# Optimization experiments

Measured on AMD Instinct MI355X. Metric: run time of the kernel, lower is better.

The kernel has to match this reference:

```python
import jax, jax.numpy as jnp
import numpy as np

B, H, S, DK, DV = 2, 16, 2048, 64, 64


def setup_inputs() -> dict:
    key = jax.random.key(0)
    kq, kk, kv, km = jax.random.split(key, 4)
    Q = jax.random.normal(kq, (B, H, S, DK), dtype=jnp.float32)
    K = jax.random.normal(kk, (B, H, S, DK), dtype=jnp.float32)
    V = jax.random.normal(kv, (B, H, S, DV), dtype=jnp.float32)
    attn_mask = jax.random.randint(km, (B, H, S, S), 0, 2).astype(jnp.bool_)
    return {
        "Q": Q, "K": K, "V": V, "attn_mask": attn_mask,
        "d_model": 1024, "n_layers": 6, "n_heads": H,
        "d_k": DK, "d_v": DV, "d_ff": 4096,
    }


def reference(Q, K, V, attn_mask, d_model, n_layers, n_heads, d_k, d_v, d_ff):
    # scores: [B, H, S, S] = Q K^T / sqrt(d_k)
    scale = 1.0 / np.sqrt(d_k).astype(np.float32)
    scores = jnp.einsum('bhqd,bhkd->bhqk', Q, K) * scale
    scores = jnp.where(attn_mask, jnp.asarray(-1e9, scores.dtype), scores)
    attn = jax.nn.softmax(scores, axis=-1)
    context = jnp.einsum('bhqk,bhkd->bhqd', attn, V)
    return (context, attn)
```

## Files before the change

### kernel.cpp

```cpp
#include <hip/hip_runtime.h>
#include <hip/hip_fp16.h>

#define S_LEN 2048
#define DKV 64
#define NBH 32
#define CTX_ELEMS ((size_t)NBH * S_LEN * DKV)

using half8 = __attribute__((ext_vector_type(8))) _Float16;
using half4 = __attribute__((ext_vector_type(4))) _Float16;
using f32x4 = __attribute__((ext_vector_type(4))) float;
using u32x4 = __attribute__((ext_vector_type(4))) unsigned int;

#define MFMA16x32(a, b, c) __builtin_amdgcn_mfma_f32_16x16x32_f16((a), (b), (c), 0, 0, 0)

__global__ void detect_mask_kernel(const unsigned char* __restrict__ mask,
                                   int* __restrict__ flag) {
  __shared__ int nz0s, nzos;
  if (threadIdx.x == 0) { nz0s = 0; nzos = 0; }
  __syncthreads();
  const u32x4* m = (const u32x4*)mask;
  unsigned int a0 = 0, ao = 0;
  for (int i = threadIdx.x; i < 8192; i += 512) {
    u32x4 v = m[i];
#pragma unroll
    for (int j = 0; j < 4; j++) {
      a0 |= v[j] & 0xffu;
      ao |= v[j] & 0xffffff00u;
    }
  }
  if (a0) atomicAdd(&nz0s, 1);
  if (ao) atomicAdd(&nzos, 1);
  __syncthreads();
  if (threadIdx.x == 0) *flag = (nz0s > 0 && nzos > 0) ? 0 : 1;
}

#define PACK_B 2048
#define CONV_B 128
#define NF4 (NBH * S_LEN * DKV / 4)

__global__ void fused_pre_kernel(const void* __restrict__ maskv,
                                 const int* __restrict__ flag,
                                 unsigned int* __restrict__ bits,
                                 const float* __restrict__ Q, _Float16* __restrict__ QH,
                                 const float* __restrict__ K, _Float16* __restrict__ KH,
                                 const float* __restrict__ V, _Float16* __restrict__ VT) {
  __shared__ unsigned char nib[256];
  __shared__ _Float16 t[64][68];
  const int bidx = blockIdx.x;
  const int tid = threadIdx.x;

  if (bidx < PACK_B) {
    const bool w4 = (*flag) != 0;
    const unsigned int* m32 = (const unsigned int*)maskv;
    if (w4) {
      const int w = tid >> 6;
      const int lane = tid & 63;
      for (int it = 0; it < 64; ++it) {
        const size_t wb = ((size_t)bidx * 64 + it) * 1024 + (size_t)w * 256;
        u32x4 v = __builtin_nontemporal_load((const u32x4*)(m32 + wb + lane * 4));
        unsigned int x = ((v[0] ? 1u : 0u) | (v[1] ? 2u : 0u) |
                          (v[2] ? 4u : 0u) | (v[3] ? 8u : 0u)) << ((lane & 7) * 4);
        x |= __shfl_xor(x, 1, 64);
        x |= __shfl_xor(x, 2, 64);
        x |= __shfl_xor(x, 4, 64);
        if ((lane & 7) == 0)
          bits[(wb >> 5) + (lane >> 3)] = x;
      }
    } else {
      for (int it = 0; it < 64; ++it) {
        const size_t e0 = ((size_t)bidx * 64 + it) * 1024;
        const size_t ei = e0 + (size_t)tid * 4;
        unsigned int b = __builtin_nontemporal_load(m32 + (ei >> 2));
        unsigned int nv = ((b & 0xffu) ? 1u : 0u) | ((b & 0xff00u) ? 2u : 0u) |
                          ((b & 0xff0000u) ? 4u : 0u) | ((b & 0xff000000u) ? 8u : 0u);
        __syncthreads();
        nib[tid] = (unsigned char)nv;
        __syncthreads();
        if (tid < 32) {
          unsigned int dw = 0;
#pragma unroll
          for (int tt = 0; tt < 8; ++tt)
            dw |= ((unsigned int)nib[tid * 8 + tt]) << (tt * 4);
          bits[(e0 >> 5) + tid] = dw;
        }
      }
    }
  } else if (bidx < PACK_B + 2 * CONV_B) {
    const bool isQ = bidx < PACK_B + CONV_B;
    const int cb = bidx - (isQ ? PACK_B : PACK_B + CONV_B);
    const float* src = isQ ? Q : K;
    _Float16* dst = isQ ? QH : KH;
    const float scale = isQ ? 0.125f : 1.0f;
    for (int i = cb * 256 + tid; i < NF4; i += CONV_B * 256) {
      f32x4 v = *(const f32x4*)(src + (size_t)i * 4);
      half4 h;
#pragma unroll
      for (int j = 0; j < 4; j++) h[j] = (_Float16)(v[j] * scale);
      *(half4*)(dst + (size_t)i * 4) = h;
    }
  } else {
    const int tIdx = bidx - (PACK_B + 2 * CONV_B);
    const int bh = tIdx >> 5;
    const int k0 = (tIdx & 31) * 64;
    const float* Vb = V + ((size_t)bh * S_LEN + k0) * DKV;
#pragma unroll
    for (int it = 0; it < 4; it++) {
      int idx = tid + it * 256;
      int kl = idx >> 4;
      int dq = (idx & 15) * 4;
      f32x4 v = *(const f32x4*)(Vb + (size_t)kl * DKV + dq);
#pragma unroll
      for (int j = 0; j < 4; j++) t[kl][dq + j] = (_Float16)v[j];
    }
    __syncthreads();
    _Float16* VTb = VT + (size_t)bh * DKV * S_LEN;
#pragma unroll
    for (int it = 0; it < 4; it++) {
      int idx = tid + it * 256;
      int d = idx >> 4;
      int kq = (idx & 15) * 4;
      half4 h;
#pragma unroll
      for (int j = 0; j < 4; j++) h[j] = t[kq + j][d];
      *(half4*)(VTb + (size_t)d * S_LEN + k0 + kq) = h;
    }
  }
}

#define LOADF(S, KT) { \
  const _Float16* kp_ = Kb + ((size_t)((KT) * 32 + c)) * DKV + g * 8; \
  k00##S = *(const half8*)kp_; \
  k01##S = *(const half8*)(kp_ + 32); \
  k10##S = *(const half8*)(kp_ + 16 * DKV); \
  k11##S = *(const half8*)(kp_ + 16 * DKV + 32); }

#define P1SUB(KT, S) { \
  unsigned int mwA[4], mwB[4]; \
  _Pragma("unroll") for (int e = 0; e < 4; e++) { \
    mwA[e] = bq[(size_t)(g * 4 + e) * (S_LEN / 32) + (KT)]; \
    mwB[e] = bq[(size_t)(16 + g * 4 + e) * (S_LEN / 32) + (KT)]; } \
  f32x4 acA0 = (f32x4)0.0f, acA1 = (f32x4)0.0f; \
  f32x4 acB0 = (f32x4)0.0f, acB1 = (f32x4)0.0f; \
  acA0 = MFMA16x32(aA0, k00##S, acA0); \
  acA0 = MFMA16x32(aA1, k01##S, acA0); \
  acB0 = MFMA16x32(aB0, k00##S, acB0); \
  acB0 = MFMA16x32(aB1, k01##S, acB0); \
  acA1 = MFMA16x32(aA0, k10##S, acA1); \
  acA1 = MFMA16x32(aA1, k11##S, acA1); \
  acB1 = MFMA16x32(aB0, k10##S, acB1); \
  acB1 = MFMA16x32(aB1, k11##S, acB1); \
  _Pragma("unroll") for (int e = 0; e < 4; e++) { \
    float pA0 = ((mwA[e] >> c) & 1u) ? 0.0f : __expf(acA0[e]); \
    float pA1 = ((mwA[e] >> (16 + c)) & 1u) ? 0.0f : __expf(acA1[e]); \
    float pB0 = ((mwB[e] >> c) & 1u) ? 0.0f : __expf(acB0[e]); \
    float pB1 = ((mwB[e] >> (16 + c)) & 1u) ? 0.0f : __expf(acB1[e]); \
    ZsA[e] += pA0 + pA1; \
    ZsB[e] += pB0 + pB1; } }

#define P2SUB(KT, S) { \
  unsigned int mwA[4], mwB[4]; \
  _Pragma("unroll") for (int e = 0; e < 4; e++) { \
    mwA[e] = bq[(size_t)(g * 4 + e) * (S_LEN / 32) + (KT)]; \
    mwB[e] = bq[(size_t)(16 + g * 4 + e) * (S_LEN / 32) + (KT)]; } \
  half8 vb0 = *(const half8*)(Vb + (size_t)(0 * 16 + c) * S_LEN + (KT) * 32 + g * 8); \
  half8 vb1 = *(const half8*)(Vb + (size_t)(1 * 16 + c) * S_LEN + (KT) * 32 + g * 8); \
  half8 vb2 = *(const half8*)(Vb + (size_t)(2 * 16 + c) * S_LEN + (KT) * 32 + g * 8); \
  half8 vb3 = *(const half8*)(Vb + (size_t)(3 * 16 + c) * S_LEN + (KT) * 32 + g * 8); \
  f32x4 acA0 = (f32x4)0.0f, acA1 = (f32x4)0.0f; \
  f32x4 acB0 = (f32x4)0.0f, acB1 = (f32x4)0.0f; \
  acA0 = MFMA16x32(aA0, k00##S, acA0); \
  acA0 = MFMA16x32(aA1, k01##S, acA0); \
  acB0 = MFMA16x32(aB0, k00##S, acB0); \
  acB0 = MFMA16x32(aB1, k01##S, acB0); \
  acA1 = MFMA16x32(aA0, k10##S, acA1); \
  acA1 = MFMA16x32(aA1, k11##S, acA1); \
  acB1 = MFMA16x32(aB0, k10##S, acB1); \
  acB1 = MFMA16x32(aB1, k11##S, acB1); \
  _Pragma("unroll") for (int e = 0; e < 4; e++) { \
    float pA0 = ((mwA[e] >> c) & 1u) ? 0.0f : __expf(acA0[e] - lZA[e]); \
    float pA1 = ((mwA[e] >> (16 + c)) & 1u) ? 0.0f : __expf(acA1[e] - lZA[e]); \
    float pB0 = ((mwB[e] >> c) & 1u) ? 0.0f : __expf(acB0[e] - lZB[e]); \
    float pB1 = ((mwB[e] >> (16 + c)) & 1u) ? 0.0f : __expf(acB1[e] - lZB[e]); \
    pbuf[w][g * 4 + e][c] = (_Float16)pA0; \
    pbuf[w][g * 4 + e][16 + c] = (_Float16)pA1; \
    pbuf[w][16 + g * 4 + e][c] = (_Float16)pB0; \
    pbuf[w][16 + g * 4 + e][16 + c] = (_Float16)pB1; } \
  half8 paA = *(const half8*)&pbuf[w][c][g * 8]; \
  half8 paB = *(const half8*)&pbuf[w][16 + c][g * 8]; \
  _Pragma("unroll") for (int s = 0; s < 4; s++) { \
    const int r = (lane >> 3) + s * 8; \
    const int c4 = (lane & 7) * 4; \
    half4 h = *(const half4*)&pbuf[w][r][c4]; \
    f32x4 o; \
    _Pragma("unroll") for (int j = 0; j < 4; j++) o[j] = (float)h[j]; \
    __builtin_nontemporal_store(o, \
        (f32x4*)(attn_base + (size_t)r * S_LEN + (KT) * 32 + c4)); } \
  ctxA[0] = MFMA16x32(paA, vb0, ctxA[0]); \
  ctxB[0] = MFMA16x32(paB, vb0, ctxB[0]); \
  ctxA[1] = MFMA16x32(paA, vb1, ctxA[1]); \
  ctxB[1] = MFMA16x32(paB, vb1, ctxB[1]); \
  ctxA[2] = MFMA16x32(paA, vb2, ctxA[2]); \
  ctxB[2] = MFMA16x32(paB, vb2, ctxB[2]); \
  ctxA[3] = MFMA16x32(paA, vb3, ctxA[3]); \
  ctxB[3] = MFMA16x32(paB, vb3, ctxB[3]); }

__global__ __launch_bounds__(512, 2)
void attn_v10_kernel(const _Float16* __restrict__ QH, const _Float16* __restrict__ KH,
                     const _Float16* __restrict__ VT, const unsigned int* __restrict__ bits,
                     float* __restrict__ out) {
  __shared__ __align__(16) _Float16 pbuf[8][32][40];
  __shared__ float zbuf[4][2][32];
  __shared__ __align__(16) float cbuf[4][32][64];

  const int tid = threadIdx.x;
  const int w = tid >> 6;
  const int lane = tid & 63;
  const int g = lane >> 4;
  const int c = lane & 15;
  const int tb = w >> 1;
  const int half = w & 1;

  const int phys = blockIdx.x;
  const int orig = (phys & 7) * 64 + (phys >> 3);
  const int tile = orig * 4 + tb;
  const int bh = tile >> 6;
  const int q0 = (tile & 63) << 5;

  const _Float16* qpA = QH + ((size_t)(bh * S_LEN + q0 + c)) * DKV + g * 8;
  const half8 aA0 = *(const half8*)qpA;
  const half8 aA1 = *(const half8*)(qpA + 32);
  const _Float16* qpB = qpA + 16 * DKV;
  const half8 aB0 = *(const half8*)qpB;
  const half8 aB1 = *(const half8*)(qpB + 32);

  const _Float16* Kb = KH + (size_t)bh * S_LEN * DKV;
  const unsigned int* bq = bits + ((size_t)(bh * S_LEN + q0)) * (S_LEN / 32);

  float ZsA[4] = {0.0f, 0.0f, 0.0f, 0.0f};
  float ZsB[4] = {0.0f, 0.0f, 0.0f, 0.0f};

  const int kt0 = half * 32;
  half8 k00a, k01a, k10a, k11a, k00b, k01b, k10b, k11b;

  LOADF(a, kt0);
  for (int sp = 0; sp < 16; ++sp) {
    const int s0 = kt0 + sp * 2;
    LOADF(b, s0 + 1);
    P1SUB(s0, a);
    if (sp < 15) LOADF(a, s0 + 2);
    P1SUB(s0 + 1, b);
  }

#pragma unroll
  for (int off = 1; off < 16; off <<= 1) {
#pragma unroll
    for (int e = 0; e < 4; e++) {
      ZsA[e] += __shfl_xor(ZsA[e], off, 64);
      ZsB[e] += __shfl_xor(ZsB[e], off, 64);
    }
  }
  if (c == 0) {
#pragma unroll
    for (int e = 0; e < 4; e++) {
      zbuf[tb][half][g * 4 + e] = ZsA[e];
      zbuf[tb][half][16 + g * 4 + e] = ZsB[e];
    }
  }
  __syncthreads();
  float lZA[4], lZB[4];
#pragma unroll
  for (int e = 0; e < 4; e++) {
    lZA[e] = __logf(zbuf[tb][0][g * 4 + e] + zbuf[tb][1][g * 4 + e]);
    lZB[e] = __logf(zbuf[tb][0][16 + g * 4 + e] + zbuf[tb][1][16 + g * 4 + e]);
  }

  f32x4 ctxA[4], ctxB[4];
#pragma unroll
  for (int nn = 0; nn < 4; nn++) { ctxA[nn] = (f32x4)0.0f; ctxB[nn] = (f32x4)0.0f; }

  const _Float16* Vb = VT + (size_t)bh * DKV * S_LEN;
  float* attn_base = out + CTX_ELEMS + ((size_t)(bh * S_LEN + q0)) * S_LEN;

  LOADF(a, kt0);
  for (int sp = 0; sp < 16; ++sp) {
    const int s0 = kt0 + sp * 2;
    LOADF(b, s0 + 1);
    P2SUB(s0, a);
    if (sp < 15) LOADF(a, s0 + 2);
    P2SUB(s0 + 1, b);
  }

  __syncthreads();
  if (half == 1) {
#pragma unroll
    for (int nn = 0; nn < 4; nn++) {
#pragma unroll
      for (int e = 0; e < 4; e++) {
        cbuf[tb][g * 4 + e][nn * 16 + c] = ctxA[nn][e];
        cbuf[tb][16 + g * 4 + e][nn * 16 + c] = ctxB[nn][e];
      }
    }
  }
  __syncthreads();
  if (half == 0) {
    float* cb = out + ((size_t)(bh * S_LEN + q0)) * DKV;
#pragma unroll
    for (int nn = 0; nn < 4; nn++) {
#pragma unroll
      for (int e = 0; e < 4; e++) {
        float vA = ctxA[nn][e] + cbuf[tb][g * 4 + e][nn * 16 + c];
        float vB = ctxB[nn][e] + cbuf[tb][16 + g * 4 + e][nn * 16 + c];
        __builtin_nontemporal_store(vA, cb + (size_t)(g * 4 + e) * DKV + nn * 16 + c);
        __builtin_nontemporal_store(vB, cb + (size_t)(16 + g * 4 + e) * DKV + nn * 16 + c);
      }
    }
  }
}

__global__ __launch_bounds__(512, 1)
void attn_slow_kernel(const float* __restrict__ Q, const float* __restrict__ K,
                      const float* __restrict__ V, const void* __restrict__ maskv,
                      float* __restrict__ out, const int* __restrict__ flag) {
  __shared__ __align__(16) unsigned char smem[16 * 2056 * 2];
  __shared__ float redm[8][16];
  __shared__ float reds[8][16];
  _Float16 (*P)[2056] = (_Float16 (*)[2056])smem;

  const int bh = blockIdx.y;
  const int q0 = blockIdx.x << 4;
  const int tid = threadIdx.x;
  const int w = tid >> 6;
  const int lane = tid & 63;
  const int g = lane >> 4;
  const int c = lane & 15;
  const int k0 = w << 8;

  const bool mask_w = (*flag) != 0;
  const unsigned char* m8 = (const unsigned char*)maskv;
  const unsigned int* m32 = (const unsigned int*)maskv;

  const float* Qb = Q + ((size_t)bh * S_LEN + q0) * DKV;
  const float* Kb = K + (size_t)bh * S_LEN * DKV;
  const float* Vb = V + (size_t)bh * S_LEN * DKV;
  const size_t mbase = ((size_t)bh * S_LEN + q0) * S_LEN;
  float* ctx_out = out + ((size_t)bh * S_LEN + q0) * DKV;
  float* attn_out = out + CTX_ELEMS + mbase;

  half8 a0, a1;
  {
    const float* qrow = Qb + (size_t)c * DKV + g * 8;
    f32x4 x0 = *(const f32x4*)(qrow);
    f32x4 x1 = *(const f32x4*)(qrow + 4);
    f32x4 y0 = *(const f32x4*)(qrow + 32);
    f32x4 y1 = *(const f32x4*)(qrow + 36);
#pragma unroll
    for (int j = 0; j < 4; j++) {
      a0[j] = (_Float16)x0[j]; a0[4 + j] = (_Float16)x1[j];
      a1[j] = (_Float16)y0[j]; a1[4 + j] = (_Float16)y1[j];
    }
  }

  f32x4 acc[16];
#pragma unroll
  for (int n = 0; n < 16; n++) acc[n] = (f32x4)0.0f;
#pragma unroll
  for (int n = 0; n < 16; n++) {
    const float* kr = Kb + (size_t)(k0 + n * 16 + c) * DKV + g * 8;
    f32x4 x0 = *(const f32x4*)(kr);
    f32x4 x1 = *(const f32x4*)(kr + 4);
    f32x4 y0 = *(const f32x4*)(kr + 32);
    f32x4 y1 = *(const f32x4*)(kr + 36);
    half8 b0, b1;
#pragma unroll
    for (int j = 0; j < 4; j++) {
      b0[j] = (_Float16)x0[j]; b0[4 + j] = (_Float16)x1[j];
      b1[j] = (_Float16)y0[j]; b1[4 + j] = (_Float16)y1[j];
    }
    acc[n] = MFMA16x32(a0, b0, acc[n]);
    acc[n] = MFMA16x32(a1, b1, acc[n]);
  }

  float mx[4] = {-1e9f, -1e9f, -1e9f, -1e9f};
#pragma unroll
  for (int n = 0; n < 16; n++) {
    const int kc = k0 + n * 16 + c;
#pragma unroll
    for (int e = 0; e < 4; e++) {
      const size_t mi = mbase + (size_t)(g * 4 + e) * S_LEN + kc;
      bool masked;
      if (mask_w) masked = (__builtin_nontemporal_load(&m32[mi]) != 0u);
      else        masked = (__builtin_nontemporal_load(&m8[mi]) != 0);
      float s = masked ? -1e9f : acc[n][e] * 0.125f;
      acc[n][e] = s;
      mx[e] = fmaxf(mx[e], s);
    }
  }
#pragma unroll
  for (int off = 1; off < 16; off <<= 1) {
#pragma unroll
    for (int e = 0; e < 4; e++)
      mx[e] = fmaxf(mx[e], __shfl_xor(mx[e], off, 64));
  }
  if (c == 0) {
#pragma unroll
    for (int e = 0; e < 4; e++) redm[w][g * 4 + e] = mx[e];
  }
  __syncthreads();
  float m[4], sm[4];
#pragma unroll
  for (int e = 0; e < 4; e++) {
    float v = redm[0][g * 4 + e];
#pragma unroll
    for (int ww = 1; ww < 8; ww++) v = fmaxf(v, redm[ww][g * 4 + e]);
    m[e] = v;
    sm[e] = 0.0f;
  }
#pragma unroll
  for (int n = 0; n < 16; n++) {
#pragma unroll
    for (int e = 0; e < 4; e++) {
      float p = __expf(acc[n][e] - m[e]);
      acc[n][e] = p;
      sm[e] += p;
    }
  }
#pragma unroll
  for (int off = 1; off < 16; off <<= 1) {
#pragma unroll
    for (int e = 0; e < 4; e++) sm[e] += __shfl_xor(sm[e], off, 64);
  }
  if (c == 0) {
#pragma unroll
    for (int e = 0; e < 4; e++) reds[w][g * 4 + e] = sm[e];
  }
  __syncthreads();
  float inv[4];
#pragma unroll
  for (int e = 0; e < 4; e++) {
    float z = 0.0f;
#pragma unroll
    for (int ww = 0; ww < 8; ww++) z += reds[ww][g * 4 + e];
    inv[e] = 1.0f / z;
  }
#pragma unroll
  for (int n = 0; n < 16; n++) {
    const int kc = k0 + n * 16 + c;
#pragma unroll
    for (int e = 0; e < 4; e++) {
      float v = acc[n][e] * inv[e];
      __builtin_nontemporal_store(v, &attn_out[(size_t)(g * 4 + e) * S_LEN + kc]);
      P[g * 4 + e][kc] = (_Float16)v;
    }
  }
  __syncthreads();

  f32x4 ctx[4];
#pragma unroll
  for (int n = 0; n < 4; n++) ctx[n] = (f32x4)0.0f;
  for (int ks = 0; ks < 8; ks++) {
    const int kb = k0 + ks * 32;
    half8 pa = *(const half8*)&P[c][kb + g * 8];
#pragma unroll
    for (int n = 0; n < 4; n++) {
      const float* vp = Vb + (size_t)(kb + g * 8) * DKV + n * 16 + c;
      half8 vb;
#pragma unroll
      for (int j = 0; j < 8; j++) vb[j] = (_Float16)vp[(size_t)j * DKV];
      ctx[n] = MFMA16x32(pa, vb, ctx[n]);
    }
  }
  __syncthreads();

  float* red2 = (float*)smem;
#pragma unroll
  for (int n = 0; n < 4; n++) {
#pragma unroll
    for (int e = 0; e < 4; e++)
      red2[((w * 16) + g * 4 + e) * 64 + n * 16 + c] = ctx[n][e];
  }
  __syncthreads();
  for (int i = tid; i < 16 * 64; i += 512) {
    int q = i >> 6, d = i & 63;
    float ssum = 0.0f;
#pragma unroll
    for (int ww = 0; ww < 8; ww++) ssum += red2[((ww * 16) + q) * 64 + d];
    ctx_out[(size_t)q * DKV + d] = ssum;
  }
}

extern "C" void kernel_launch(void* const* d_in, const int* in_sizes, int n_in,
                              void* d_out, int out_size, void* d_ws, size_t ws_size,
                              hipStream_t stream) {
  (void)in_sizes; (void)n_in; (void)out_size;
  const float* Q = (const float*)d_in[0];
  const float* K = (const float*)d_in[1];
  const float* V = (const float*)d_in[2];
  const void* mask = d_in[3];

  const size_t HBYTES = (size_t)NBH * S_LEN * DKV * sizeof(_Float16);
  const size_t BITBYTES = (size_t)NBH * S_LEN * (S_LEN / 32) * 4;
  const size_t NEED = 256 + 3 * HBYTES + BITBYTES;

  int* flag = (int*)d_ws;
  hipLaunchKernelGGL(detect_mask_kernel, dim3(1), dim3(512), 0, stream,
                     (const unsigned char*)mask, flag);

  if (ws_size >= NEED) {
    _Float16* QH = (_Float16*)((char*)d_ws + 256);
    _Float16* KH = (_Float16*)((char*)d_ws + 256 + HBYTES);
    _Float16* VT = (_Float16*)((char*)d_ws + 256 + 2 * HBYTES);
    unsigned int* bits = (unsigned int*)((char*)d_ws + 256 + 3 * HBYTES);
    hipLaunchKernelGGL(fused_pre_kernel,
                       dim3(PACK_B + 2 * CONV_B + (S_LEN / 64) * NBH), dim3(256), 0, stream,
                       mask, flag, bits, Q, QH, K, KH, V, VT);
    hipLaunchKernelGGL(attn_v10_kernel, dim3(512), dim3(512), 0, stream,
                       QH, KH, VT, bits, (float*)d_out);
  } else {
    hipLaunchKernelGGL(attn_slow_kernel, dim3(128, 32), dim3(512), 0, stream,
                       Q, K, V, mask, (float*)d_out, flag);
  }
}
```

Before: 350.3 us.

## Split normalizer pass into separate kernel with finer query tiles

Moves the first pass (softmax denominator computation) out of the fused attention kernel into its own kernel that handles 16-row query tiles over 1024 blocks at higher occupancy, writing log-normalizers to workspace. The second kernel reads lnZ and only does the P/attn-write/PV pass. Also reorders the PV MFMAs before the attention-probability stores inside the inner step. This is meant to raise parallelism and occupancy for the compute-bound first pass and to shrink the main kernel's register footprint. In exchange it adds a kernel launch and a small global round-trip for lnZ.

```diff
diff --git a/kernel.cpp b/kernel.cpp
--- a/kernel.cpp
+++ b/kernel.cpp
@@ -127,35 +127,91 @@
   }
 }
 
+#define L1F(S, KT) { \
+  const _Float16* kp_ = Kb + ((size_t)((KT) * 32 + c)) * DKV + g * 8; \
+  j00##S = *(const half8*)kp_; \
+  j01##S = *(const half8*)(kp_ + 32); \
+  j10##S = *(const half8*)(kp_ + 16 * DKV); \
+  j11##S = *(const half8*)(kp_ + 16 * DKV + 32); }
+
+#define P1S(KT, S) { \
+  unsigned int mw[4]; \
+  _Pragma("unroll") for (int e = 0; e < 4; e++) \
+    mw[e] = bq[(size_t)(g * 4 + e) * (S_LEN / 32) + (KT)]; \
+  f32x4 acc0 = (f32x4)0.0f, acc1 = (f32x4)0.0f; \
+  acc0 = MFMA16x32(a0, j00##S, acc0); \
+  acc0 = MFMA16x32(a1, j01##S, acc0); \
+  acc1 = MFMA16x32(a0, j10##S, acc1); \
+  acc1 = MFMA16x32(a1, j11##S, acc1); \
+  _Pragma("unroll") for (int e = 0; e < 4; e++) { \
+    float p0 = ((mw[e] >> c) & 1u) ? 0.0f : __expf(acc0[e]); \
+    float p1 = ((mw[e] >> (16 + c)) & 1u) ? 0.0f : __expf(acc1[e]); \
+    Zs[e] += p0 + p1; } }
+
+__global__ __launch_bounds__(512, 3)
+void pass1_kernel(const _Float16* __restrict__ QH, const _Float16* __restrict__ KH,
+                  const unsigned int* __restrict__ bits, float* __restrict__ lnZ) {
+  __shared__ float zbuf[4][2][16];
+
+  const int tid = threadIdx.x;
+  const int w = tid >> 6;
+  const int lane = tid & 63;
+  const int g = lane >> 4;
+  const int c = lane & 15;
+  const int tb = w >> 1;
+  const int half = w & 1;
+
+  const int phys = blockIdx.x;
+  const int orig = (phys & 7) * 128 + (phys >> 3);
+  const int tile = orig * 4 + tb;
+  const int bh = tile >> 7;
+  const int q0 = (tile & 127) << 4;
+
+  const _Float16* qp = QH + ((size_t)(bh * S_LEN + q0 + c)) * DKV + g * 8;
+  const half8 a0 = *(const half8*)qp;
+  const half8 a1 = *(const half8*)(qp + 32);
+
+  const _Float16* Kb = KH + (size_t)bh * S_LEN * DKV;
+  const unsigned int* bq = bits + ((size_t)(bh * S_LEN + q0)) * (S_LEN / 32);
+
+  float Zs[4] = {0.0f, 0.0f, 0.0f, 0.0f};
+  const int kt0 = half * 32;
+  half8 j00a, j01a, j10a, j11a, j00b, j01b, j10b, j11b;
+
+  L1F(a, kt0);
+  for (int sp = 0; sp < 16; ++sp) {
+    const int s0 = kt0 + sp * 2;
+    L1F(b, s0 + 1);
+    P1S(s0, a);
+    if (sp < 15) L1F(a, s0 + 2);
+    P1S(s0 + 1, b);
+  }
+
+#pragma unroll
+  for (int off = 1; off < 16; off <<= 1) {
+#pragma unroll
+    for (int e = 0; e < 4; e++) Zs[e] += __shfl_xor(Zs[e], off, 64);
+  }
+  if (c == 0) {
+#pragma unroll
+    for (int e = 0; e < 4; e++) zbuf[tb][half][g * 4 + e] = Zs[e];
+  }
+  __syncthreads();
+  if (half == 0 && c == 0) {
+#pragma unroll
+    for (int e = 0; e < 4; e++) {
+      float z = zbuf[tb][0][g * 4 + e] + zbuf[tb][1][g * 4 + e];
+      lnZ[(size_t)bh * S_LEN + q0 + g * 4 + e] = __logf(z);
+    }
+  }
+}
+
 #define LOADF(S, KT) { \
   const _Float16* kp_ = Kb + ((size_t)((KT) * 32 + c)) * DKV + g * 8; \
   k00##S = *(const half8*)kp_; \
   k01##S = *(const half8*)(kp_ + 32); \
   k10##S = *(const half8*)(kp_ + 16 * DKV); \
   k11##S = *(const half8*)(kp_ + 16 * DKV + 32); }
-
-#define P1SUB(KT, S) { \
-  unsigned int mwA[4], mwB[4]; \
-  _Pragma("unroll") for (int e = 0; e < 4; e++) { \
-    mwA[e] = bq[(size_t)(g * 4 + e) * (S_LEN / 32) + (KT)]; \
-    mwB[e] = bq[(size_t)(16 + g * 4 + e) * (S_LEN / 32) + (KT)]; } \
-  f32x4 acA0 = (f32x4)0.0f, acA1 = (f32x4)0.0f; \
-  f32x4 acB0 = (f32x4)0.0f, acB1 = (f32x4)0.0f; \
-  acA0 = MFMA16x32(aA0, k00##S, acA0); \
-  acA0 = MFMA16x32(aA1, k01##S, acA0); \
-  acB0 = MFMA16x32(aB0, k00##S, acB0); \
-  acB0 = MFMA16x32(aB1, k01##S, acB0); \
-  acA1 = MFMA16x32(aA0, k10##S, acA1); \
-  acA1 = MFMA16x32(aA1, k11##S, acA1); \
-  acB1 = MFMA16x32(aB0, k10##S, acB1); \
-  acB1 = MFMA16x32(aB1, k11##S, acB1); \
-  _Pragma("unroll") for (int e = 0; e < 4; e++) { \
-    float pA0 = ((mwA[e] >> c) & 1u) ? 0.0f : __expf(acA0[e]); \
-    float pA1 = ((mwA[e] >> (16 + c)) & 1u) ? 0.0f : __expf(acA1[e]); \
-    float pB0 = ((mwB[e] >> c) & 1u) ? 0.0f : __expf(acB0[e]); \
-    float pB1 = ((mwB[e] >> (16 + c)) & 1u) ? 0.0f : __expf(acB1[e]); \
-    ZsA[e] += pA0 + pA1; \
-    ZsB[e] += pB0 + pB1; } }
 
 #define P2SUB(KT, S) { \
   unsigned int mwA[4], mwB[4]; \
@@ -187,6 +243,14 @@
     pbuf[w][16 + g * 4 + e][16 + c] = (_Float16)pB1; } \
   half8 paA = *(const half8*)&pbuf[w][c][g * 8]; \
   half8 paB = *(const half8*)&pbuf[w][16 + c][g * 8]; \
+  ctxA[0] = MFMA16x32(paA, vb0, ctxA[0]); \
+  ctxB[0] = MFMA16x32(paB, vb0, ctxB[0]); \
+  ctxA[1] = MFMA16x32(paA, vb1, ctxA[1]); \
+  ctxB[1] = MFMA16x32(paB, vb1, ctxB[1]); \
+  ctxA[2] = MFMA16x32(paA, vb2, ctxA[2]); \
+  ctxB[2] = MFMA16x32(paB, vb2, ctxB[2]); \
+  ctxA[3] = MFMA16x32(paA, vb3, ctxA[3]); \
+  ctxB[3] = MFMA16x32(paB, vb3, ctxB[3]); \
   _Pragma("unroll") for (int s = 0; s < 4; s++) { \
     const int r = (lane >> 3) + s * 8; \
     const int c4 = (lane & 7) * 4; \
@@ -194,22 +258,13 @@
     f32x4 o; \
     _Pragma("unroll") for (int j = 0; j < 4; j++) o[j] = (float)h[j]; \
     __builtin_nontemporal_store(o, \
-        (f32x4*)(attn_base + (size_t)r * S_LEN + (KT) * 32 + c4)); } \
-  ctxA[0] = MFMA16x32(paA, vb0, ctxA[0]); \
-  ctxB[0] = MFMA16x32(paB, vb0, ctxB[0]); \
-  ctxA[1] = MFMA16x32(paA, vb1, ctxA[1]); \
-  ctxB[1] = MFMA16x32(paB, vb1, ctxB[1]); \
-  ctxA[2] = MFMA16x32(paA, vb2, ctxA[2]); \
-  ctxB[2] = MFMA16x32(paB, vb2, ctxB[2]); \
-  ctxA[3] = MFMA16x32(paA, vb3, ctxA[3]); \
-  ctxB[3] = MFMA16x32(paB, vb3, ctxB[3]); }
+        (f32x4*)(attn_base + (size_t)r * S_LEN + (KT) * 32 + c4)); } }
 
 __global__ __launch_bounds__(512, 2)
-void attn_v10_kernel(const _Float16* __restrict__ QH, const _Float16* __restrict__ KH,
-                     const _Float16* __restrict__ VT, const unsigned int* __restrict__ bits,
-                     float* __restrict__ out) {
+void pass2_kernel(const _Float16* __restrict__ QH, const _Float16* __restrict__ KH,
+                  const _Float16* __restrict__ VT, const unsigned int* __restrict__ bits,
+                  const float* __restrict__ lnZ, float* __restrict__ out) {
   __shared__ __align__(16) _Float16 pbuf[8][32][40];
-  __shared__ float zbuf[4][2][32];
   __shared__ __align__(16) float cbuf[4][32][64];
 
   const int tid = threadIdx.x;
@@ -236,50 +291,23 @@
   const _Float16* Kb = KH + (size_t)bh * S_LEN * DKV;
   const unsigned int* bq = bits + ((size_t)(bh * S_LEN + q0)) * (S_LEN / 32);
 
-  float ZsA[4] = {0.0f, 0.0f, 0.0f, 0.0f};
-  float ZsB[4] = {0.0f, 0.0f, 0.0f, 0.0f};
+  float lZA[4], lZB[4];
+  const float* zrow = lnZ + (size_t)bh * S_LEN + q0;
+#pragma unroll
+  for (int e = 0; e < 4; e++) {
+    lZA[e] = zrow[g * 4 + e];
+    lZB[e] = zrow[16 + g * 4 + e];
+  }
+
+  f32x4 ctxA[4], ctxB[4];
+#pragma unroll
+  for (int nn = 0; nn < 4; nn++) { ctxA[nn] = (f32x4)0.0f; ctxB[nn] = (f32x4)0.0f; }
+
+  const _Float16* Vb = VT + (size_t)bh * DKV * S_LEN;
+  float* attn_base = out + CTX_ELEMS + ((size_t)(bh * S_LEN + q0)) * S_LEN;
 
   const int kt0 = half * 32;
   half8 k00a, k01a, k10a, k11a, k00b, k01b, k10b, k11b;
-
-  LOADF(a, kt0);
-  for (int sp = 0; sp < 16; ++sp) {
-    const int s0 = kt0 + sp * 2;
-    LOADF(b, s0 + 1);
-    P1SUB(s0, a);
-    if (sp < 15) LOADF(a, s0 + 2);
-    P1SUB(s0 + 1, b);
-  }
-
-#pragma unroll
-  for (int off = 1; off < 16; off <<= 1) {
-#pragma unroll
-    for (int e = 0; e < 4; e++) {
-      ZsA[e] += __shfl_xor(ZsA[e], off, 64);
-      ZsB[e] += __shfl_xor(ZsB[e], off, 64);
-    }
-  }
-  if (c == 0) {
-#pragma unroll
-    for (int e = 0; e < 4; e++) {
-      zbuf[tb][half][g * 4 + e] = ZsA[e];
-      zbuf[tb][half][16 + g * 4 + e] = ZsB[e];
-    }
-  }
-  __syncthreads();
-  float lZA[4], lZB[4];
-#pragma unroll
-  for (int e = 0; e < 4; e++) {
-    lZA[e] = __logf(zbuf[tb][0][g * 4 + e] + zbuf[tb][1][g * 4 + e]);
-    lZB[e] = __logf(zbuf[tb][0][16 + g * 4 + e] + zbuf[tb][1][16 + g * 4 + e]);
-  }
-
-  f32x4 ctxA[4], ctxB[4];
-#pragma unroll
-  for (int nn = 0; nn < 4; nn++) { ctxA[nn] = (f32x4)0.0f; ctxB[nn] = (f32x4)0.0f; }
-
-  const _Float16* Vb = VT + (size_t)bh * DKV * S_LEN;
-  float* attn_base = out + CTX_ELEMS + ((size_t)(bh * S_LEN + q0)) * S_LEN;
 
   LOADF(a, kt0);
   for (int sp = 0; sp < 16; ++sp) {
@@ -499,7 +527,8 @@
 
   const size_t HBYTES = (size_t)NBH * S_LEN * DKV * sizeof(_Float16);
   const size_t BITBYTES = (size_t)NBH * S_LEN * (S_LEN / 32) * 4;
-  const size_t NEED = 256 + 3 * HBYTES + BITBYTES;
+  const size_t LNZBYTES = (size_t)NBH * S_LEN * 4;
+  const size_t NEED = 256 + 3 * HBYTES + BITBYTES + LNZBYTES;
 
   int* flag = (int*)d_ws;
   hipLaunchKernelGGL(detect_mask_kernel, dim3(1), dim3(512), 0, stream,
@@ -510,11 +539,14 @@
     _Float16* KH = (_Float16*)((char*)d_ws + 256 + HBYTES);
     _Float16* VT = (_Float16*)((char*)d_ws + 256 + 2 * HBYTES);
     unsigned int* bits = (unsigned int*)((char*)d_ws + 256 + 3 * HBYTES);
+    float* lnZ = (float*)((char*)d_ws + 256 + 3 * HBYTES + BITBYTES);
     hipLaunchKernelGGL(fused_pre_kernel,
                        dim3(PACK_B + 2 * CONV_B + (S_LEN / 64) * NBH), dim3(256), 0, stream,
                        mask, flag, bits, Q, QH, K, KH, V, VT);
-    hipLaunchKernelGGL(attn_v10_kernel, dim3(512), dim3(512), 0, stream,
-                       QH, KH, VT, bits, (float*)d_out);
+    hipLaunchKernelGGL(pass1_kernel, dim3(1024), dim3(512), 0, stream,
+                       QH, KH, bits, lnZ);
+    hipLaunchKernelGGL(pass2_kernel, dim3(512), dim3(512), 0, stream,
+                       QH, KH, VT, bits, lnZ, (float*)d_out);
   } else {
     hipLaunchKernelGGL(attn_slow_kernel, dim3(128, 32), dim3(512), 0, stream,
                        Q, K, V, mask, (float*)d_out, flag);
```

After: 398.6 us. 13.8% more time.

## Pack mask into per-lane MFMA-layout words, fuse 4-byte mask packing into pass one

Applied to the files above, without the earlier changes.

Replaces the row-major bitmask with per-lane 32-bit words laid out to match the MFMA accumulator layout, so each lane loads one word per k-pair instead of eight scattered words. When the mask is stored as 4-byte elements, the packing is moved out of the pre-kernel and done inside the first softmax pass, which reads the raw mask and writes the packed words for reuse in pass two. This removes a separate full pass over the mask, but adds strided raw-mask reads inside the compute loop.

```diff
diff --git a/kernel.cpp b/kernel.cpp
--- a/kernel.cpp
+++ b/kernel.cpp
@@ -40,50 +40,43 @@
 
 __global__ void fused_pre_kernel(const void* __restrict__ maskv,
                                  const int* __restrict__ flag,
-                                 unsigned int* __restrict__ bits,
+                                 unsigned int* __restrict__ mb,
                                  const float* __restrict__ Q, _Float16* __restrict__ QH,
                                  const float* __restrict__ K, _Float16* __restrict__ KH,
                                  const float* __restrict__ V, _Float16* __restrict__ VT) {
-  __shared__ unsigned char nib[256];
   __shared__ _Float16 t[64][68];
   const int bidx = blockIdx.x;
   const int tid = threadIdx.x;
 
   if (bidx < PACK_B) {
-    const bool w4 = (*flag) != 0;
-    const unsigned int* m32 = (const unsigned int*)maskv;
-    if (w4) {
-      const int w = tid >> 6;
-      const int lane = tid & 63;
-      for (int it = 0; it < 64; ++it) {
-        const size_t wb = ((size_t)bidx * 64 + it) * 1024 + (size_t)w * 256;
-        u32x4 v = __builtin_nontemporal_load((const u32x4*)(m32 + wb + lane * 4));
-        unsigned int x = ((v[0] ? 1u : 0u) | (v[1] ? 2u : 0u) |
-                          (v[2] ? 4u : 0u) | (v[3] ? 8u : 0u)) << ((lane & 7) * 4);
-        x |= __shfl_xor(x, 1, 64);
-        x |= __shfl_xor(x, 2, 64);
-        x |= __shfl_xor(x, 4, 64);
-        if ((lane & 7) == 0)
-          bits[(wb >> 5) + (lane >> 3)] = x;
+    if ((*flag) != 0) return;
+    const unsigned char* m8 = (const unsigned char*)maskv;
+    const int bh = bidx >> 6;
+    const int q0 = (bidx & 63) << 5;
+    const unsigned char* m8b = m8 + (size_t)(bh * S_LEN + q0) * S_LEN;
+    for (int idx = tid; idx < 2048; idx += 256) {
+      const int lane = idx & 63;
+      const int sph = idx >> 6;
+      const int hf = sph >> 4;
+      const int sp = sph & 15;
+      const int g = lane >> 4;
+      const int c = lane & 15;
+      unsigned int mword = 0;
+#pragma unroll
+      for (int s01 = 0; s01 < 2; ++s01) {
+        const int kt = hf * 32 + sp * 2 + s01;
+        const unsigned char* mp = m8b + (size_t)(g * 4) * S_LEN + kt * 32 + c;
+        unsigned int t16 = 0;
+#pragma unroll
+        for (int e = 0; e < 4; e++) {
+          if (mp[(size_t)e * S_LEN]) t16 |= 1u << e;
+          if (mp[(size_t)e * S_LEN + 16]) t16 |= 1u << (4 + e);
+          if (mp[(size_t)(16 + e) * S_LEN]) t16 |= 1u << (8 + e);
+          if (mp[(size_t)(16 + e) * S_LEN + 16]) t16 |= 1u << (12 + e);
+        }
+        mword |= t16 << (16 * s01);
       }
-    } else {
-      for (int it = 0; it < 64; ++it) {
-        const size_t e0 = ((size_t)bidx * 64 + it) * 1024;
-        const size_t ei = e0 + (size_t)tid * 4;
-        unsigned int b = __builtin_nontemporal_load(m32 + (ei >> 2));
-        unsigned int nv = ((b & 0xffu) ? 1u : 0u) | ((b & 0xff00u) ? 2u : 0u) |
-                          ((b & 0xff0000u) ? 4u : 0u) | ((b & 0xff000000u) ? 8u : 0u);
-        __syncthreads();
-        nib[tid] = (unsigned char)nv;
-        __syncthreads();
-        if (tid < 32) {
-          unsigned int dw = 0;
-#pragma unroll
-          for (int tt = 0; tt < 8; ++tt)
-            dw |= ((unsigned int)nib[tid * 8 + tt]) << (tt * 4);
-          bits[(e0 >> 5) + tid] = dw;
-        }
-      }
+      mb[(((size_t)bidx * 2 + hf) * 16 + sp) * 64 + lane] = mword;
     }
   } else if (bidx < PACK_B + 2 * CONV_B) {
     const bool isQ = bidx < PACK_B + CONV_B;
@@ -134,11 +127,18 @@
   k10##S = *(const half8*)(kp_ + 16 * DKV); \
   k11##S = *(const half8*)(kp_ + 16 * DKV + 32); }
 
-#define P1SUB(KT, S) { \
-  unsigned int mwA[4], mwB[4]; \
+#define P1TESTW(KT, SH) { \
+  const unsigned int* mp_ = m32b + (size_t)(KT) * 32 + c; \
+  unsigned int t16_ = 0; \
   _Pragma("unroll") for (int e = 0; e < 4; e++) { \
-    mwA[e] = bq[(size_t)(g * 4 + e) * (S_LEN / 32) + (KT)]; \
-    mwB[e] = bq[(size_t)(16 + g * 4 + e) * (S_LEN / 32) + (KT)]; } \
+    if (mp_[(size_t)e * S_LEN] != 0u)             t16_ |= 1u << e; \
+    if (mp_[(size_t)e * S_LEN + 16] != 0u)        t16_ |= 1u << (4 + e); \
+    if (mp_[(size_t)(16 + e) * S_LEN] != 0u)      t16_ |= 1u << (8 + e); \
+    if (mp_[(size_t)(16 + e) * S_LEN + 16] != 0u) t16_ |= 1u << (12 + e); \
+  } \
+  mword |= t16_ << (SH); }
+
+#define P1COMP(S, SH) { \
   f32x4 acA0 = (f32x4)0.0f, acA1 = (f32x4)0.0f; \
   f32x4 acB0 = (f32x4)0.0f, acB1 = (f32x4)0.0f; \
   acA0 = MFMA16x32(aA0, k00##S, acA0); \
@@ -150,18 +150,14 @@
   acB1 = MFMA16x32(aB0, k10##S, acB1); \
   acB1 = MFMA16x32(aB1, k11##S, acB1); \
   _Pragma("unroll") for (int e = 0; e < 4; e++) { \
-    float pA0 = ((mwA[e] >> c) & 1u) ? 0.0f : __expf(acA0[e]); \
-    float pA1 = ((mwA[e] >> (16 + c)) & 1u) ? 0.0f : __expf(acA1[e]); \
-    float pB0 = ((mwB[e] >> c) & 1u) ? 0.0f : __expf(acB0[e]); \
-    float pB1 = ((mwB[e] >> (16 + c)) & 1u) ? 0.0f : __expf(acB1[e]); \
+    float pA0 = ((mword >> ((SH) + e)) & 1u) ? 0.0f : __expf(acA0[e]); \
+    float pA1 = ((mword >> ((SH) + 4 + e)) & 1u) ? 0.0f : __expf(acA1[e]); \
+    float pB0 = ((mword >> ((SH) + 8 + e)) & 1u) ? 0.0f : __expf(acB0[e]); \
+    float pB1 = ((mword >> ((SH) + 12 + e)) & 1u) ? 0.0f : __expf(acB1[e]); \
     ZsA[e] += pA0 + pA1; \
     ZsB[e] += pB0 + pB1; } }
 
-#define P2SUB(KT, S) { \
-  unsigned int mwA[4], mwB[4]; \
-  _Pragma("unroll") for (int e = 0; e < 4; e++) { \
-    mwA[e] = bq[(size_t)(g * 4 + e) * (S_LEN / 32) + (KT)]; \
-    mwB[e] = bq[(size_t)(16 + g * 4 + e) * (S_LEN / 32) + (KT)]; } \
+#define P2COMP(KT, S, SH) { \
   half8 vb0 = *(const half8*)(Vb + (size_t)(0 * 16 + c) * S_LEN + (KT) * 32 + g * 8); \
   half8 vb1 = *(const half8*)(Vb + (size_t)(1 * 16 + c) * S_LEN + (KT) * 32 + g * 8); \
   half8 vb2 = *(const half8*)(Vb + (size_t)(2 * 16 + c) * S_LEN + (KT) * 32 + g * 8); \
@@ -177,10 +173,10 @@
   acB1 = MFMA16x32(aB0, k10##S, acB1); \
   acB1 = MFMA16x32(aB1, k11##S, acB1); \
   _Pragma("unroll") for (int e = 0; e < 4; e++) { \
-    float pA0 = ((mwA[e] >> c) & 1u) ? 0.0f : __expf(acA0[e] - lZA[e]); \
-    float pA1 = ((mwA[e] >> (16 + c)) & 1u) ? 0.0f : __expf(acA1[e] - lZA[e]); \
-    float pB0 = ((mwB[e] >> c) & 1u) ? 0.0f : __expf(acB0[e] - lZB[e]); \
-    float pB1 = ((mwB[e] >> (16 + c)) & 1u) ? 0.0f : __expf(acB1[e] - lZB[e]); \
+    float pA0 = ((mword >> ((SH) + e)) & 1u) ? 0.0f : __expf(acA0[e] - lZA[e]); \
+    float pA1 = ((mword >> ((SH) + 4 + e)) & 1u) ? 0.0f : __expf(acA1[e] - lZA[e]); \
+    float pB0 = ((mword >> ((SH) + 8 + e)) & 1u) ? 0.0f : __expf(acB0[e] - lZB[e]); \
+    float pB1 = ((mword >> ((SH) + 12 + e)) & 1u) ? 0.0f : __expf(acB1[e] - lZB[e]); \
     pbuf[w][g * 4 + e][c] = (_Float16)pA0; \
     pbuf[w][g * 4 + e][16 + c] = (_Float16)pA1; \
     pbuf[w][16 + g * 4 + e][c] = (_Float16)pB0; \
@@ -205,8 +201,9 @@
   ctxB[3] = MFMA16x32(paB, vb3, ctxB[3]); }
 
 __global__ __launch_bounds__(512, 2)
-void attn_v10_kernel(const _Float16* __restrict__ QH, const _Float16* __restrict__ KH,
-                     const _Float16* __restrict__ VT, const unsigned int* __restrict__ bits,
+void attn_v12_kernel(const _Float16* __restrict__ QH, const _Float16* __restrict__ KH,
+                     const _Float16* __restrict__ VT, const void* __restrict__ maskv,
+                     unsigned int* __restrict__ mb, const int* __restrict__ flag,
                      float* __restrict__ out) {
   __shared__ __align__(16) _Float16 pbuf[8][32][40];
   __shared__ float zbuf[4][2][32];
@@ -226,6 +223,10 @@
   const int bh = tile >> 6;
   const int q0 = (tile & 63) << 5;
 
+  const bool mask_w = (*flag) != 0;
+  const unsigned int* m32b = (const unsigned int*)maskv +
+                             (size_t)(bh * S_LEN + q0 + g * 4) * S_LEN;
+
   const _Float16* qpA = QH + ((size_t)(bh * S_LEN + q0 + c)) * DKV + g * 8;
   const half8 aA0 = *(const half8*)qpA;
   const half8 aA1 = *(const half8*)(qpA + 32);
@@ -234,7 +235,7 @@
   const half8 aB1 = *(const half8*)(qpB + 32);
 
   const _Float16* Kb = KH + (size_t)bh * S_LEN * DKV;
-  const unsigned int* bq = bits + ((size_t)(bh * S_LEN + q0)) * (S_LEN / 32);
+  const size_t mbbase = ((size_t)(tile * 2 + half) * 16) * 64 + lane;
 
   float ZsA[4] = {0.0f, 0.0f, 0.0f, 0.0f};
   float ZsB[4] = {0.0f, 0.0f, 0.0f, 0.0f};
@@ -246,9 +247,18 @@
   for (int sp = 0; sp < 16; ++sp) {
     const int s0 = kt0 + sp * 2;
     LOADF(b, s0 + 1);
-    P1SUB(s0, a);
+    unsigned int mword;
+    if (mask_w) {
+      mword = 0;
+      P1TESTW(s0, 0);
+      P1TESTW(s0 + 1, 16);
+    } else {
+      mword = mb[mbbase + (size_t)sp * 64];
+    }
+    P1COMP(a, 0);
     if (sp < 15) LOADF(a, s0 + 2);
-    P1SUB(s0 + 1, b);
+    P1COMP(b, 16);
+    if (mask_w) mb[mbbase + (size_t)sp * 64] = mword;
   }
 
 #pragma unroll
@@ -285,9 +295,10 @@
   for (int sp = 0; sp < 16; ++sp) {
     const int s0 = kt0 + sp * 2;
     LOADF(b, s0 + 1);
-    P2SUB(s0, a);
+    const unsigned int mword = mb[mbbase + (size_t)sp * 64];
+    P2COMP(s0, a, 0);
     if (sp < 15) LOADF(a, s0 + 2);
-    P2SUB(s0 + 1, b);
+    P2COMP(s0 + 1, b, 16);
   }
 
   __syncthreads();
@@ -498,8 +509,8 @@
   const void* mask = d_in[3];
 
   const size_t HBYTES = (size_t)NBH * S_LEN * DKV * sizeof(_Float16);
-  const size_t BITBYTES = (size_t)NBH * S_LEN * (S_LEN / 32) * 4;
-  const size_t NEED = 256 + 3 * HBYTES + BITBYTES;
+  const size_t MBBYTES = (size_t)2048 * 2 * 16 * 64 * 4;
+  const size_t NEED = 256 + 3 * HBYTES + MBBYTES;
 
   int* flag = (int*)d_ws;
   hipLaunchKernelGGL(detect_mask_kernel, dim3(1), dim3(512), 0, stream,
@@ -509,12 +520,12 @@
     _Float16* QH = (_Float16*)((char*)d_ws + 256);
     _Float16* KH = (_Float16*)((char*)d_ws + 256 + HBYTES);
     _Float16* VT = (_Float16*)((char*)d_ws + 256 + 2 * HBYTES);
-    unsigned int* bits = (unsigned int*)((char*)d_ws + 256 + 3 * HBYTES);
+    unsigned int* mb = (unsigned int*)((char*)d_ws + 256 + 3 * HBYTES);
     hipLaunchKernelGGL(fused_pre_kernel,
                        dim3(PACK_B + 2 * CONV_B + (S_LEN / 64) * NBH), dim3(256), 0, stream,
-                       mask, flag, bits, Q, QH, K, KH, V, VT);
-    hipLaunchKernelGGL(attn_v10_kernel, dim3(512), dim3(512), 0, stream,
-                       QH, KH, VT, bits, (float*)d_out);
+                       mask, flag, mb, Q, QH, K, KH, V, VT);
+    hipLaunchKernelGGL(attn_v12_kernel, dim3(512), dim3(512), 0, stream,
+                       QH, KH, VT, mask, mb, flag, (float*)d_out);
   } else {
     hipLaunchKernelGGL(attn_slow_kernel, dim3(128, 32), dim3(512), 0, stream,
                        Q, K, V, mask, (float*)d_out, flag);
```

Measured after the change: 425.2 us. 1.21x slower.
